# Kernel optimization log

Hardware: AMD Instinct MI355X
Metric: run time of the kernel (lower is better)

Reference implementation:

```python
import jax, jax.numpy as jnp
import numpy as np

N_RAYS = 131072
N_NODES = 524288
ENC_DEPTH = 8
ENC_DIM = 16
N_POINTS = 8
IN_DIM = N_POINTS * ENC_DEPTH * ENC_DIM  # 1024
INNER = 64


def setup_inputs() -> dict:
    key = jax.random.key(0)
    ks = jax.random.split(key, 9)
    orig = jax.random.uniform(ks[0], (N_RAYS, 3), dtype=jnp.float32)
    end = jax.random.uniform(ks[1], (N_RAYS, 3), dtype=jnp.float32)
    history = jax.random.randint(ks[2], (N_RAYS, ENC_DEPTH), 0, N_NODES, dtype=jnp.int32).astype(jnp.int64)
    nodes_min = jax.random.uniform(ks[3], (N_NODES, 3), dtype=jnp.float32)
    # extents strictly positive (module replaces 0 extents with 0.5)
    nodes_extent = jax.random.uniform(ks[4], (N_NODES, 3), dtype=jnp.float32) + 0.1
    emb = jax.random.normal(ks[5], (N_NODES, 8 * ENC_DIM), dtype=jnp.float32) * 0.1
    W1 = jax.random.normal(ks[6], (IN_DIM, INNER), dtype=jnp.float32) * (1.0 / np.sqrt(IN_DIM))
    W2 = jax.random.normal(ks[7], (INNER, INNER), dtype=jnp.float32) * (1.0 / np.sqrt(INNER))
    W3 = jax.random.normal(ks[8], (INNER, 2), dtype=jnp.float32) * (1.0 / np.sqrt(INNER))
    return {"orig": orig, "end": end, "history": history, "nodes_min": nodes_min,
            "nodes_extent": nodes_extent, "emb": emb, "W1": W1, "W2": W2, "W3": W3}


def _net_forward(orig, end, history, nodes_min, nodes_extent, emb, W1, W2, W3):
    n = orig.shape[0]
    d = history.shape[1]
    # gather per-ray, per-depth node data (irregular access)
    nmin = nodes_min[history]          # (n, d, 3)
    ext = nodes_extent[history]        # (n, d, 3)
    po = jnp.clip((orig[:, None, :] - nmin) / ext, 0.0, 1.0)  # (n, d, 3)
    pe = jnp.clip((end[:, None, :] - nmin) / ext, 0.0, 1.0)
    ts = jnp.linspace(0.0, 1.0, N_POINTS, dtype=orig.dtype)
    pts = po[:, :, None, :] + (pe - po)[:, :, None, :] * ts[None, None, :, None]  # (n, d, P, 3)
    xd, yd, zd = pts[..., 0], pts[..., 1], pts[..., 2]
    # corner weights in the same order as bbox_feature.chunk(8): 000,100,010,001,101,011,110,111
    w = jnp.stack([
        (1 - xd) * (1 - yd) * (1 - zd),
        xd * (1 - yd) * (1 - zd),
        (1 - xd) * yd * (1 - zd),
        (1 - xd) * (1 - yd) * zd,
        xd * (1 - yd) * zd,
        (1 - xd) * yd * zd,
        xd * yd * (1 - zd),
        xd * yd * zd,
    ], axis=-1)                                    # (n, d, P, 8)
    corners = emb[history].reshape(n, d, 8, ENC_DIM)  # (n, d, 8, F)
    feat = jnp.einsum('ndpk,ndkf->ndpf', w, corners)  # (n, d, P, F)
    feat = feat.reshape(n, d * N_POINTS * ENC_DIM)    # concat over depth
    h = jax.nn.relu(feat @ W1)
    h = jax.nn.relu(h @ W2)
    a = h @ W3                                        # (n, 2)
    lengths = jnp.linalg.norm(end - orig, axis=-1)
    pred_cls = a[:, 0]
    pred_dist = a[:, 1] * lengths
    return jnp.stack([pred_cls, pred_dist], axis=-1)  # (n, 2)


def reference(orig, end, history, nodes_min, nodes_extent, emb, W1, W2, W3):
    return _net_forward(orig, end, history, nodes_min, nodes_extent, emb, W1, W2, W3)
```

## Files before the change

kernel.cpp:

```cpp
#include <hip/hip_runtime.h>
#include <hip/hip_bf16.h>
#include <cstdint>

#define ENC_DEPTH 8
#define RAYS_PER_BLOCK 64
#define THREADS 512

typedef __attribute__((ext_vector_type(8))) short bf16x8;
typedef __attribute__((ext_vector_type(4))) float f32x4;

__device__ __forceinline__ unsigned short f2bf(float x) {
    union { float f; unsigned u; } v; v.f = x;
    unsigned r = v.u + 0x7fffu + ((v.u >> 16) & 1u);
    return (unsigned short)(r >> 16);
}
__device__ __forceinline__ float bf2f(unsigned short h) {
    union { unsigned u; float f; } v; v.u = ((unsigned)h) << 16;
    return v.f;
}
__device__ __forceinline__ float clamp01(float x) {
    return fminf(fmaxf(x, 0.0f), 1.0f);
}

__global__ __launch_bounds__(THREADS, 4) void nbvh_kernel(
    const float* __restrict__ orig, const float* __restrict__ endp,
    const int* __restrict__ hist, const float* __restrict__ nodes_min,
    const float* __restrict__ nodes_extent, const float* __restrict__ emb,
    const float* __restrict__ W1, const float* __restrict__ W2,
    const float* __restrict__ W3, float* __restrict__ out)
{
    __shared__ int hist_s[RAYS_PER_BLOCK * ENC_DEPTH];
    __shared__ float oe_s[RAYS_PER_BLOCK * 6];
    __shared__ __align__(16) unsigned short corners_s[RAYS_PER_BLOCK * 136];
    __shared__ __align__(16) unsigned short feat_s[RAYS_PER_BLOCK * 136];
    __shared__ __align__(16) unsigned short w1t_s[64 * 136];
    __shared__ float h1_s[RAYS_PER_BLOCK * 65];

    const int t = threadIdx.x;
    const int r0 = blockIdx.x * RAYS_PER_BLOCK;
    const int wave = t >> 6;
    const int lane = t & 63;
    const int ray_c = t >> 3, k_c = t & 7;
    const int rl = t >> 2, cg = (t & 3) << 4;

    hist_s[t] = hist[r0 * ENC_DEPTH + t];
    if (t < RAYS_PER_BLOCK * 3) {
        int ray = t / 3, c = t - ray * 3;
        oe_s[ray * 6 + c]     = orig[(r0 + ray) * 3 + c];
        oe_s[ray * 6 + 3 + c] = endp[(r0 + ray) * 3 + c];
    }
    asm volatile("s_waitcnt lgkmcnt(0)" ::: "memory");

    int node0 = hist_s[ray_c << 3];
    const float4* ep = (const float4*)(emb + ((size_t)node0 << 7) + (k_c << 4));
    float4 pf0 = ep[0], pf1 = ep[1], pf2 = ep[2], pf3 = ep[3];
    const float4* wp = (const float4*)(W1 + (size_t)rl * 64 + cg);
    float4 wf0 = wp[0], wf1 = wp[1], wf2 = wp[2], wf3 = wp[3];
    float nm0 = nodes_min[node0 * 3 + 0];
    float nm1 = nodes_min[node0 * 3 + 1];
    float nm2 = nodes_min[node0 * 3 + 2];
    float ex0 = nodes_extent[node0 * 3 + 0];
    float ex1 = nodes_extent[node0 * 3 + 1];
    float ex2 = nodes_extent[node0 * 3 + 2];

    f32x4 acc0 = {0.f, 0.f, 0.f, 0.f};
    f32x4 acc1 = {0.f, 0.f, 0.f, 0.f};
    const int m0 = (wave >> 1) * 16;
    const int n0 = (wave & 1) * 32;

    __builtin_amdgcn_s_barrier();
    asm volatile("" ::: "memory");

    float nn0 = 0.f, nn1 = 0.f, nn2 = 0.f, en0 = 0.f, en1 = 0.f, en2 = 0.f;

    for (int d = 0; d < ENC_DEPTH; ++d) {
        {
            float e[16];
            e[0]=pf0.x; e[1]=pf0.y; e[2]=pf0.z; e[3]=pf0.w;
            e[4]=pf1.x; e[5]=pf1.y; e[6]=pf1.z; e[7]=pf1.w;
            e[8]=pf2.x; e[9]=pf2.y; e[10]=pf2.z; e[11]=pf2.w;
            e[12]=pf3.x; e[13]=pf3.y; e[14]=pf3.z; e[15]=pf3.w;
            unsigned short* cb = corners_s + ray_c * 136 + k_c;
            #pragma unroll
            for (int f = 0; f < 16; ++f) cb[f << 3] = f2bf(e[f]);
        }
        {
            float a[16];
            a[0]=wf0.x; a[1]=wf0.y; a[2]=wf0.z; a[3]=wf0.w;
            a[4]=wf1.x; a[5]=wf1.y; a[6]=wf1.z; a[7]=wf1.w;
            a[8]=wf2.x; a[9]=wf2.y; a[10]=wf2.z; a[11]=wf2.w;
            a[12]=wf3.x; a[13]=wf3.y; a[14]=wf3.z; a[15]=wf3.w;
            unsigned short* wb = w1t_s + (size_t)cg * 136 + rl;
            #pragma unroll
            for (int i = 0; i < 16; ++i) wb[i * 136] = f2bf(a[i]);
        }
        if (d < ENC_DEPTH - 1) {
            int node1 = hist_s[(ray_c << 3) + d + 1];
            const float4* ep2 = (const float4*)(emb + ((size_t)node1 << 7) + (k_c << 4));
            pf0 = ep2[0]; pf1 = ep2[1]; pf2 = ep2[2]; pf3 = ep2[3];
            const float4* wp2 = (const float4*)(W1 + (size_t)((d + 1) * 128 + rl) * 64 + cg);
            wf0 = wp2[0]; wf1 = wp2[1]; wf2 = wp2[2]; wf3 = wp2[3];
            nn0 = nodes_min[node1 * 3 + 0];
            nn1 = nodes_min[node1 * 3 + 1];
            nn2 = nodes_min[node1 * 3 + 2];
            en0 = nodes_extent[node1 * 3 + 0];
            en1 = nodes_extent[node1 * 3 + 1];
            en2 = nodes_extent[node1 * 3 + 2];
        }

        {
            const float* oe = oe_s + ray_c * 6;
            float rx = __builtin_amdgcn_rcpf(ex0);
            float ry = __builtin_amdgcn_rcpf(ex1);
            float rz = __builtin_amdgcn_rcpf(ex2);
            float po0 = clamp01((oe[0] - nm0) * rx);
            float po1 = clamp01((oe[1] - nm1) * ry);
            float po2 = clamp01((oe[2] - nm2) * rz);
            float pe0 = clamp01((oe[3] - nm0) * rx);
            float pe1 = clamp01((oe[4] - nm1) * ry);
            float pe2 = clamp01((oe[5] - nm2) * rz);
            float tt = (float)k_c * (1.0f / 7.0f);
            float x = po0 + (pe0 - po0) * tt;
            float y = po1 + (pe1 - po1) * tt;
            float z = po2 + (pe2 - po2) * tt;
            float ox = 1.f - x, oy = 1.f - y, oz = 1.f - z;
            float w[8];
            w[0] = ox * oy * oz;  w[1] = x * oy * oz;
            w[2] = ox * y * oz;   w[3] = ox * oy * z;
            w[4] = x * oy * z;    w[5] = ox * y * z;
            w[6] = x * y * oz;    w[7] = x * y * z;
            const unsigned short* cbase = corners_s + ray_c * 136;
            bf16x8 f0v, f1v;
            #pragma unroll
            for (int f = 0; f < 16; ++f) {
                bf16x8 cv = *(const bf16x8*)(cbase + (f << 3));
                float acc = 0.f;
                #pragma unroll
                for (int k = 0; k < 8; ++k)
                    acc = fmaf(w[k], bf2f((unsigned short)cv[k]), acc);
                unsigned short h = f2bf(acc);
                if (f < 8) f0v[f] = (short)h; else f1v[f - 8] = (short)h;
            }
            unsigned short* fb = feat_s + ray_c * 136 + (k_c << 4);
            *(bf16x8*)fb = f0v;
            *(bf16x8*)(fb + 8) = f1v;
        }

        asm volatile("s_waitcnt lgkmcnt(0)" ::: "memory");
        __builtin_amdgcn_s_barrier();
        asm volatile("" ::: "memory");

        {
            int q = lane >> 4, c = lane & 15;
            #pragma unroll
            for (int kk = 0; kk < 4; ++kk) {
                int koff = kk * 32 + q * 8;
                bf16x8 af = *(const bf16x8*)(feat_s + (m0 + c) * 136 + koff);
                bf16x8 b0 = *(const bf16x8*)(w1t_s + (n0 + c) * 136 + koff);
                bf16x8 b1 = *(const bf16x8*)(w1t_s + (n0 + 16 + c) * 136 + koff);
                acc0 = __builtin_amdgcn_mfma_f32_16x16x32_bf16(af, b0, acc0, 0, 0, 0);
                acc1 = __builtin_amdgcn_mfma_f32_16x16x32_bf16(af, b1, acc1, 0, 0, 0);
            }
        }

        asm volatile("s_waitcnt lgkmcnt(0)" ::: "memory");
        __builtin_amdgcn_s_barrier();
        asm volatile("" ::: "memory");

        if (d < ENC_DEPTH - 1) {
            nm0 = nn0; nm1 = nn1; nm2 = nn2;
            ex0 = en0; ex1 = en1; ex2 = en2;
        }
    }

    {
        int colb = lane & 15, rq = (lane >> 4) << 2;
        #pragma unroll
        for (int r = 0; r < 4; ++r) {
            h1_s[(m0 + rq + r) * 65 + n0 + colb]      = fmaxf(acc0[r], 0.f);
            h1_s[(m0 + rq + r) * 65 + n0 + 16 + colb] = fmaxf(acc1[r], 0.f);
        }
    }
    __syncthreads();

    float* h2_s = (float*)corners_s;
    {
        int ray = t >> 3, jg = (t & 7) << 3;
        float s[8];
        #pragma unroll
        for (int j = 0; j < 8; ++j) s[j] = 0.f;
        const float* hrow = h1_s + ray * 65;
        #pragma unroll 8
        for (int i = 0; i < 64; ++i) {
            float hv = hrow[i];
            const float4* wr = (const float4*)(W2 + (i << 6) + jg);
            float4 wa = wr[0], wb = wr[1];
            s[0] = fmaf(hv, wa.x, s[0]); s[1] = fmaf(hv, wa.y, s[1]);
            s[2] = fmaf(hv, wa.z, s[2]); s[3] = fmaf(hv, wa.w, s[3]);
            s[4] = fmaf(hv, wb.x, s[4]); s[5] = fmaf(hv, wb.y, s[5]);
            s[6] = fmaf(hv, wb.z, s[6]); s[7] = fmaf(hv, wb.w, s[7]);
        }
        float* hb = h2_s + ray * 66 + jg;
        #pragma unroll
        for (int j = 0; j < 8; ++j) hb[j] = fmaxf(s[j], 0.f);
    }
    __syncthreads();

    if (t < 128) {
        int ray = t >> 1, c = t & 1;
        const float* hrow = h2_s + ray * 66;
        float a = 0.f;
        #pragma unroll 16
        for (int i = 0; i < 64; ++i) a = fmaf(hrow[i], W3[i * 2 + c], a);
        if (c) {
            const float* oe = oe_s + ray * 6;
            float dx = oe[3] - oe[0], dy = oe[4] - oe[1], dz = oe[5] - oe[2];
            a *= sqrtf(dx * dx + dy * dy + dz * dz);
        }
        out[((r0 + ray) << 1) + c] = a;
    }
}

extern "C" void kernel_launch(void* const* d_in, const int* in_sizes, int n_in,
                              void* d_out, int out_size, void* d_ws, size_t ws_size,
                              hipStream_t stream) {
    const float* orig = (const float*)d_in[0];
    const float* endp = (const float*)d_in[1];
    const int*   hist = (const int*)d_in[2];
    const float* nmin = (const float*)d_in[3];
    const float* next = (const float*)d_in[4];
    const float* emb  = (const float*)d_in[5];
    const float* W1   = (const float*)d_in[6];
    const float* W2   = (const float*)d_in[7];
    const float* W3   = (const float*)d_in[8];
    float* out = (float*)d_out;
    const int n_rays = in_sizes[0] / 3;
    dim3 grid(n_rays / RAYS_PER_BLOCK);
    nbvh_kernel<<<grid, THREADS, 0, stream>>>(orig, endp, hist, nmin, next,
                                              emb, W1, W2, W3, out);
}
```

Measured before the change: 539.3 us.

## Vectorize LDS writes, drop hist/oe shared staging, stage W2 in LDS, raise occupancy

```diff
diff --git a/kernel.cpp b/kernel.cpp
--- a/kernel.cpp
+++ b/kernel.cpp
@@ -1,9 +1,8 @@
 #include <hip/hip_runtime.h>
-#include <hip/hip_bf16.h>
 #include <cstdint>
 
 #define ENC_DEPTH 8
-#define RAYS_PER_BLOCK 64
+#define RPB 64
 #define THREADS 512
 
 typedef __attribute__((ext_vector_type(8))) short bf16x8;
@@ -18,108 +17,101 @@
     union { unsigned u; float f; } v; v.u = ((unsigned)h) << 16;
     return v.f;
 }
-__device__ __forceinline__ float clamp01(float x) {
-    return fminf(fmaxf(x, 0.0f), 1.0f);
-}
-
-__global__ __launch_bounds__(THREADS, 4) void nbvh_kernel(
+__device__ __forceinline__ float clamp01(float x) { return fminf(fmaxf(x, 0.f), 1.f); }
+
+__global__ __launch_bounds__(THREADS, 6) void nbvh_kernel(
     const float* __restrict__ orig, const float* __restrict__ endp,
     const int* __restrict__ hist, const float* __restrict__ nodes_min,
     const float* __restrict__ nodes_extent, const float* __restrict__ emb,
     const float* __restrict__ W1, const float* __restrict__ W2,
     const float* __restrict__ W3, float* __restrict__ out)
 {
-    __shared__ int hist_s[RAYS_PER_BLOCK * ENC_DEPTH];
-    __shared__ float oe_s[RAYS_PER_BLOCK * 6];
-    __shared__ __align__(16) unsigned short corners_s[RAYS_PER_BLOCK * 136];
-    __shared__ __align__(16) unsigned short feat_s[RAYS_PER_BLOCK * 136];
+    __shared__ __align__(16) unsigned short corners_s[RPB * 136];
+    __shared__ __align__(16) unsigned short feat_s[RPB * 136];
     __shared__ __align__(16) unsigned short w1t_s[64 * 136];
-    __shared__ float h1_s[RAYS_PER_BLOCK * 65];
 
     const int t = threadIdx.x;
-    const int r0 = blockIdx.x * RAYS_PER_BLOCK;
-    const int wave = t >> 6;
-    const int lane = t & 63;
-    const int ray_c = t >> 3, k_c = t & 7;
-    const int rl = t >> 2, cg = (t & 3) << 4;
-
-    hist_s[t] = hist[r0 * ENC_DEPTH + t];
-    if (t < RAYS_PER_BLOCK * 3) {
-        int ray = t / 3, c = t - ray * 3;
-        oe_s[ray * 6 + c]     = orig[(r0 + ray) * 3 + c];
-        oe_s[ray * 6 + 3 + c] = endp[(r0 + ray) * 3 + c];
-    }
-    asm volatile("s_waitcnt lgkmcnt(0)" ::: "memory");
-
-    int node0 = hist_s[ray_c << 3];
-    const float4* ep = (const float4*)(emb + ((size_t)node0 << 7) + (k_c << 4));
+    const int r0 = blockIdx.x * RPB;
+    const int wave = t >> 6, lane = t & 63;
+    const int ray = t >> 3, kc = t & 7;
+
+    const float* opr = orig + (size_t)(r0 + ray) * 3;
+    const float* epr = endp + (size_t)(r0 + ray) * 3;
+    float oex = opr[0], oey = opr[1], oez = opr[2];
+    float eex = epr[0], eey = epr[1], eez = epr[2];
+
+    const int* hrow_g = hist + (size_t)(r0 + ray) * ENC_DEPTH;
+
+    int node = hrow_g[0];
+    const float4* ep = (const float4*)(emb + ((size_t)node << 7) + (kc << 4));
     float4 pf0 = ep[0], pf1 = ep[1], pf2 = ep[2], pf3 = ep[3];
-    const float4* wp = (const float4*)(W1 + (size_t)rl * 64 + cg);
-    float4 wf0 = wp[0], wf1 = wp[1], wf2 = wp[2], wf3 = wp[3];
-    float nm0 = nodes_min[node0 * 3 + 0];
-    float nm1 = nodes_min[node0 * 3 + 1];
-    float nm2 = nodes_min[node0 * 3 + 2];
-    float ex0 = nodes_extent[node0 * 3 + 0];
-    float ex1 = nodes_extent[node0 * 3 + 1];
-    float ex2 = nodes_extent[node0 * 3 + 2];
+    float w1p[16];
+    #pragma unroll
+    for (int j = 0; j < 16; ++j)
+        w1p[j] = W1[(size_t)((j >> 3) * 64 + wave * 8 + (j & 7)) * 64 + lane];
+    float nm0 = nodes_min[node * 3 + 0], nm1 = nodes_min[node * 3 + 1], nm2 = nodes_min[node * 3 + 2];
+    float ex0 = nodes_extent[node * 3 + 0], ex1 = nodes_extent[node * 3 + 1], ex2 = nodes_extent[node * 3 + 2];
 
     f32x4 acc0 = {0.f, 0.f, 0.f, 0.f};
     f32x4 acc1 = {0.f, 0.f, 0.f, 0.f};
     const int m0 = (wave >> 1) * 16;
     const int n0 = (wave & 1) * 32;
 
-    __builtin_amdgcn_s_barrier();
-    asm volatile("" ::: "memory");
-
     float nn0 = 0.f, nn1 = 0.f, nn2 = 0.f, en0 = 0.f, en1 = 0.f, en2 = 0.f;
 
     for (int d = 0; d < ENC_DEPTH; ++d) {
         {
-            float e[16];
-            e[0]=pf0.x; e[1]=pf0.y; e[2]=pf0.z; e[3]=pf0.w;
-            e[4]=pf1.x; e[5]=pf1.y; e[6]=pf1.z; e[7]=pf1.w;
-            e[8]=pf2.x; e[9]=pf2.y; e[10]=pf2.z; e[11]=pf2.w;
-            e[12]=pf3.x; e[13]=pf3.y; e[14]=pf3.z; e[15]=pf3.w;
-            unsigned short* cb = corners_s + ray_c * 136 + k_c;
-            #pragma unroll
-            for (int f = 0; f < 16; ++f) cb[f << 3] = f2bf(e[f]);
-        }
-        {
-            float a[16];
-            a[0]=wf0.x; a[1]=wf0.y; a[2]=wf0.z; a[3]=wf0.w;
-            a[4]=wf1.x; a[5]=wf1.y; a[6]=wf1.z; a[7]=wf1.w;
-            a[8]=wf2.x; a[9]=wf2.y; a[10]=wf2.z; a[11]=wf2.w;
-            a[12]=wf3.x; a[13]=wf3.y; a[14]=wf3.z; a[15]=wf3.w;
-            unsigned short* wb = w1t_s + (size_t)cg * 136 + rl;
-            #pragma unroll
-            for (int i = 0; i < 16; ++i) wb[i * 136] = f2bf(a[i]);
+            float e0 = pf0.x, e1 = pf0.y, e2 = pf0.z, e3 = pf0.w;
+            float e4 = pf1.x, e5 = pf1.y, e6 = pf1.z, e7 = pf1.w;
+            float e8 = pf2.x, e9 = pf2.y, e10 = pf2.z, e11 = pf2.w;
+            float e12 = pf3.x, e13 = pf3.y, e14 = pf3.z, e15 = pf3.w;
+            bf16x8 c0, c1;
+            c0[0] = (short)f2bf(e0);  c0[1] = (short)f2bf(e1);
+            c0[2] = (short)f2bf(e2);  c0[3] = (short)f2bf(e3);
+            c0[4] = (short)f2bf(e4);  c0[5] = (short)f2bf(e5);
+            c0[6] = (short)f2bf(e6);  c0[7] = (short)f2bf(e7);
+            c1[0] = (short)f2bf(e8);  c1[1] = (short)f2bf(e9);
+            c1[2] = (short)f2bf(e10); c1[3] = (short)f2bf(e11);
+            c1[4] = (short)f2bf(e12); c1[5] = (short)f2bf(e13);
+            c1[6] = (short)f2bf(e14); c1[7] = (short)f2bf(e15);
+            unsigned short* cb = corners_s + ray * 136 + (kc << 4);
+            *(bf16x8*)cb = c0;
+            *(bf16x8*)(cb + 8) = c1;
+        }
+        {
+            bf16x8 wv0, wv1;
+            #pragma unroll
+            for (int j = 0; j < 8; ++j) {
+                wv0[j] = (short)f2bf(w1p[j]);
+                wv1[j] = (short)f2bf(w1p[8 + j]);
+            }
+            unsigned short* wb = w1t_s + lane * 136 + wave * 8;
+            *(bf16x8*)wb = wv0;
+            *(bf16x8*)(wb + 64) = wv1;
         }
         if (d < ENC_DEPTH - 1) {
-            int node1 = hist_s[(ray_c << 3) + d + 1];
-            const float4* ep2 = (const float4*)(emb + ((size_t)node1 << 7) + (k_c << 4));
+            int node1 = hrow_g[d + 1];
+            const float4* ep2 = (const float4*)(emb + ((size_t)node1 << 7) + (kc << 4));
             pf0 = ep2[0]; pf1 = ep2[1]; pf2 = ep2[2]; pf3 = ep2[3];
-            const float4* wp2 = (const float4*)(W1 + (size_t)((d + 1) * 128 + rl) * 64 + cg);
-            wf0 = wp2[0]; wf1 = wp2[1]; wf2 = wp2[2]; wf3 = wp2[3];
-            nn0 = nodes_min[node1 * 3 + 0];
-            nn1 = nodes_min[node1 * 3 + 1];
-            nn2 = nodes_min[node1 * 3 + 2];
-            en0 = nodes_extent[node1 * 3 + 0];
-            en1 = nodes_extent[node1 * 3 + 1];
-            en2 = nodes_extent[node1 * 3 + 2];
-        }
-
-        {
-            const float* oe = oe_s + ray_c * 6;
+            const float* w1b = W1 + (size_t)(d + 1) * 128 * 64;
+            #pragma unroll
+            for (int j = 0; j < 16; ++j)
+                w1p[j] = w1b[(size_t)((j >> 3) * 64 + wave * 8 + (j & 7)) * 64 + lane];
+            nn0 = nodes_min[node1 * 3 + 0]; nn1 = nodes_min[node1 * 3 + 1]; nn2 = nodes_min[node1 * 3 + 2];
+            en0 = nodes_extent[node1 * 3 + 0]; en1 = nodes_extent[node1 * 3 + 1]; en2 = nodes_extent[node1 * 3 + 2];
+        }
+
+        {
             float rx = __builtin_amdgcn_rcpf(ex0);
             float ry = __builtin_amdgcn_rcpf(ex1);
             float rz = __builtin_amdgcn_rcpf(ex2);
-            float po0 = clamp01((oe[0] - nm0) * rx);
-            float po1 = clamp01((oe[1] - nm1) * ry);
-            float po2 = clamp01((oe[2] - nm2) * rz);
-            float pe0 = clamp01((oe[3] - nm0) * rx);
-            float pe1 = clamp01((oe[4] - nm1) * ry);
-            float pe2 = clamp01((oe[5] - nm2) * rz);
-            float tt = (float)k_c * (1.0f / 7.0f);
+            float po0 = clamp01((oex - nm0) * rx);
+            float po1 = clamp01((oey - nm1) * ry);
+            float po2 = clamp01((oez - nm2) * rz);
+            float pe0 = clamp01((eex - nm0) * rx);
+            float pe1 = clamp01((eey - nm1) * ry);
+            float pe2 = clamp01((eez - nm2) * rz);
+            float tt = (float)kc * (1.0f / 7.0f);
             float x = po0 + (pe0 - po0) * tt;
             float y = po1 + (pe1 - po1) * tt;
             float z = po2 + (pe2 - po2) * tt;
@@ -129,19 +121,27 @@
             w[2] = ox * y * oz;   w[3] = ox * oy * z;
             w[4] = x * oy * z;    w[5] = ox * y * z;
             w[6] = x * y * oz;    w[7] = x * y * z;
-            const unsigned short* cbase = corners_s + ray_c * 136;
+            float facc[16];
+            #pragma unroll
+            for (int f = 0; f < 16; ++f) facc[f] = 0.f;
+            const unsigned short* cbase = corners_s + ray * 136;
+            #pragma unroll
+            for (int k = 0; k < 8; ++k) {
+                bf16x8 cv0 = *(const bf16x8*)(cbase + (k << 4));
+                bf16x8 cv1 = *(const bf16x8*)(cbase + (k << 4) + 8);
+                #pragma unroll
+                for (int f = 0; f < 8; ++f) {
+                    facc[f]     = fmaf(w[k], bf2f((unsigned short)cv0[f]), facc[f]);
+                    facc[f + 8] = fmaf(w[k], bf2f((unsigned short)cv1[f]), facc[f + 8]);
+                }
+            }
             bf16x8 f0v, f1v;
             #pragma unroll
-            for (int f = 0; f < 16; ++f) {
-                bf16x8 cv = *(const bf16x8*)(cbase + (f << 3));
-                float acc = 0.f;
-                #pragma unroll
-                for (int k = 0; k < 8; ++k)
-                    acc = fmaf(w[k], bf2f((unsigned short)cv[k]), acc);
-                unsigned short h = f2bf(acc);
-                if (f < 8) f0v[f] = (short)h; else f1v[f - 8] = (short)h;
-            }
-            unsigned short* fb = feat_s + ray_c * 136 + (k_c << 4);
+            for (int f = 0; f < 8; ++f) {
+                f0v[f] = (short)f2bf(facc[f]);
+                f1v[f] = (short)f2bf(facc[f + 8]);
+            }
+            unsigned short* fb = feat_s + ray * 136 + (kc << 4);
             *(bf16x8*)fb = f0v;
             *(bf16x8*)(fb + 8) = f1v;
         }
@@ -167,57 +167,98 @@
         __builtin_amdgcn_s_barrier();
         asm volatile("" ::: "memory");
 
-        if (d < ENC_DEPTH - 1) {
-            nm0 = nn0; nm1 = nn1; nm2 = nn2;
-            ex0 = en0; ex1 = en1; ex2 = en2;
-        }
-    }
-
+        nm0 = nn0; nm1 = nn1; nm2 = nn2;
+        ex0 = en0; ex1 = en1; ex2 = en2;
+    }
+
+    float* h1s = (float*)feat_s;
     {
         int colb = lane & 15, rq = (lane >> 4) << 2;
         #pragma unroll
         for (int r = 0; r < 4; ++r) {
-            h1_s[(m0 + rq + r) * 65 + n0 + colb]      = fmaxf(acc0[r], 0.f);
-            h1_s[(m0 + rq + r) * 65 + n0 + 16 + colb] = fmaxf(acc1[r], 0.f);
-        }
-    }
-    __syncthreads();
-
-    float* h2_s = (float*)corners_s;
+            h1s[(m0 + rq + r) * 68 + n0 + colb]      = fmaxf(acc0[r], 0.f);
+            h1s[(m0 + rq + r) * 68 + n0 + 16 + colb] = fmaxf(acc1[r], 0.f);
+        }
+    }
+    float* w2s = (float*)w1t_s;
     {
-        int ray = t >> 3, jg = (t & 7) << 3;
-        float s[8];
+        int row = t >> 3, cg = (t & 7) << 3;
+        const float4* wr = (const float4*)(W2 + (row << 6) + cg);
+        float4 wa = wr[0], wb = wr[1];
+        *(float4*)(w2s + row * 68 + cg) = wa;
+        *(float4*)(w2s + row * 68 + cg + 4) = wb;
+    }
+    asm volatile("s_waitcnt lgkmcnt(0)" ::: "memory");
+    __builtin_amdgcn_s_barrier();
+    asm volatile("" ::: "memory");
+
+    float* h2s = (float*)corners_s;
+    {
+        int jg = (t & 7) << 3;
+        float s0 = 0.f, s1 = 0.f, s2 = 0.f, s3 = 0.f, s4 = 0.f, s5 = 0.f, s6 = 0.f, s7 = 0.f;
+        const float* hr = h1s + ray * 68;
         #pragma unroll
-        for (int j = 0; j < 8; ++j) s[j] = 0.f;
-        const float* hrow = h1_s + ray * 65;
-        #pragma unroll 8
-        for (int i = 0; i < 64; ++i) {
-            float hv = hrow[i];
-            const float4* wr = (const float4*)(W2 + (i << 6) + jg);
-            float4 wa = wr[0], wb = wr[1];
-            s[0] = fmaf(hv, wa.x, s[0]); s[1] = fmaf(hv, wa.y, s[1]);
-            s[2] = fmaf(hv, wa.z, s[2]); s[3] = fmaf(hv, wa.w, s[3]);
-            s[4] = fmaf(hv, wb.x, s[4]); s[5] = fmaf(hv, wb.y, s[5]);
-            s[6] = fmaf(hv, wb.z, s[6]); s[7] = fmaf(hv, wb.w, s[7]);
-        }
-        float* hb = h2_s + ray * 66 + jg;
+        for (int i4 = 0; i4 < 16; ++i4) {
+            float4 hv = *(const float4*)(hr + (i4 << 2));
+            const float* w0p = w2s + (i4 * 4 + 0) * 68 + jg;
+            const float* w1q = w2s + (i4 * 4 + 1) * 68 + jg;
+            const float* w2q = w2s + (i4 * 4 + 2) * 68 + jg;
+            const float* w3q = w2s + (i4 * 4 + 3) * 68 + jg;
+            float4 a0 = *(const float4*)w0p, b0 = *(const float4*)(w0p + 4);
+            float4 a1 = *(const float4*)w1q, b1 = *(const float4*)(w1q + 4);
+            float4 a2 = *(const float4*)w2q, b2 = *(const float4*)(w2q + 4);
+            float4 a3 = *(const float4*)w3q, b3 = *(const float4*)(w3q + 4);
+            s0 = fmaf(hv.x, a0.x, s0); s1 = fmaf(hv.x, a0.y, s1);
+            s2 = fmaf(hv.x, a0.z, s2); s3 = fmaf(hv.x, a0.w, s3);
+            s4 = fmaf(hv.x, b0.x, s4); s5 = fmaf(hv.x, b0.y, s5);
+            s6 = fmaf(hv.x, b0.z, s6); s7 = fmaf(hv.x, b0.w, s7);
+            s0 = fmaf(hv.y, a1.x, s0); s1 = fmaf(hv.y, a1.y, s1);
+            s2 = fmaf(hv.y, a1.z, s2); s3 = fmaf(hv.y, a1.w, s3);
+            s4 = fmaf(hv.y, b1.x, s4); s5 = fmaf(hv.y, b1.y, s5);
+            s6 = fmaf(hv.y, b1.z, s6); s7 = fmaf(hv.y, b1.w, s7);
+            s0 = fmaf(hv.z, a2.x, s0); s1 = fmaf(hv.z, a2.y, s1);
+            s2 = fmaf(hv.z, a2.z, s2); s3 = fmaf(hv.z, a2.w, s3);
+            s4 = fmaf(hv.z, b2.x, s4); s5 = fmaf(hv.z, b2.y, s5);
+            s6 = fmaf(hv.z, b2.z, s6); s7 = fmaf(hv.z, b2.w, s7);
+            s0 = fmaf(hv.w, a3.x, s0); s1 = fmaf(hv.w, a3.y, s1);
+            s2 = fmaf(hv.w, a3.z, s2); s3 = fmaf(hv.w, a3.w, s3);
+            s4 = fmaf(hv.w, b3.x, s4); s5 = fmaf(hv.w, b3.y, s5);
+            s6 = fmaf(hv.w, b3.z, s6); s7 = fmaf(hv.w, b3.w, s7);
+        }
+        float4 r1; r1.x = fmaxf(s0, 0.f); r1.y = fmaxf(s1, 0.f); r1.z = fmaxf(s2, 0.f); r1.w = fmaxf(s3, 0.f);
+        float4 r2; r2.x = fmaxf(s4, 0.f); r2.y = fmaxf(s5, 0.f); r2.z = fmaxf(s6, 0.f); r2.w = fmaxf(s7, 0.f);
+        float* hb = h2s + ray * 68 + jg;
+        *(float4*)hb = r1;
+        *(float4*)(hb + 4) = r2;
+    }
+    asm volatile("s_waitcnt lgkmcnt(0)" ::: "memory");
+    __builtin_amdgcn_s_barrier();
+    asm volatile("" ::: "memory");
+
+    if (t < 128) {
+        int ray2 = t >> 1, c = t & 1;
+        const float* hr = h2s + ray2 * 68;
+        float a = 0.f;
         #pragma unroll
-        for (int j = 0; j < 8; ++j) hb[j] = fmaxf(s[j], 0.f);
-    }
-    __syncthreads();
-
-    if (t < 128) {
-        int ray = t >> 1, c = t & 1;
-        const float* hrow = h2_s + ray * 66;
-        float a = 0.f;
-        #pragma unroll 16
-        for (int i = 0; i < 64; ++i) a = fmaf(hrow[i], W3[i * 2 + c], a);
+        for (int i4 = 0; i4 < 16; ++i4) {
+            float4 hv = *(const float4*)(hr + (i4 << 2));
+            const float4* w3p = (const float4*)(W3 + (i4 << 3));
+            float4 wa = w3p[0], wb = w3p[1];
+            if (c == 0) {
+                a = fmaf(hv.x, wa.x, a); a = fmaf(hv.y, wa.z, a);
+                a = fmaf(hv.z, wb.x, a); a = fmaf(hv.w, wb.z, a);
+            } else {
+                a = fmaf(hv.x, wa.y, a); a = fmaf(hv.y, wa.w, a);
+                a = fmaf(hv.z, wb.y, a); a = fmaf(hv.w, wb.w, a);
+            }
+        }
         if (c) {
-            const float* oe = oe_s + ray * 6;
-            float dx = oe[3] - oe[0], dy = oe[4] - oe[1], dz = oe[5] - oe[2];
+            const float* o2p = orig + (size_t)(r0 + ray2) * 3;
+            const float* e2p = endp + (size_t)(r0 + ray2) * 3;
+            float dx = e2p[0] - o2p[0], dy = e2p[1] - o2p[1], dz = e2p[2] - o2p[2];
             a *= sqrtf(dx * dx + dy * dy + dz * dz);
         }
-        out[((r0 + ray) << 1) + c] = a;
+        out[((r0 + ray2) << 1) + c] = a;
     }
 }
 
@@ -235,7 +276,7 @@
     const float* W3   = (const float*)d_in[8];
     float* out = (float*)d_out;
     const int n_rays = in_sizes[0] / 3;
-    dim3 grid(n_rays / RAYS_PER_BLOCK);
+    dim3 grid(n_rays / RPB);
     nbvh_kernel<<<grid, THREADS, 0, stream>>>(orig, endp, hist, nmin, next,
                                               emb, W1, W2, W3, out);
 }
```

Result: slower. 1.178 ms (+118.4%).
